# Kernel optimization log

Hardware: AMD Instinct MI355X
Metric: run time of the kernel (lower is better)

Reference implementation:

```python
import jax, jax.numpy as jnp
import numpy as np

B, S, HID = 1, 2048, 2048
NH, NKV, HD = 32, 8, 64  # query heads, kv heads, head dim
NEG = -1e9


def rotate_half(x):
    d = x.shape[-1] // 2
    return jnp.concatenate([-x[..., d:], x[..., :d]], axis=-1)


def setup_inputs() -> dict:
    key = jax.random.key(0)
    ks = jax.random.split(key, 8)
    hidden_states = jax.random.normal(ks[0], (B, S, HID), dtype=jnp.float32)
    # RoPE angles: realistic cos/sin tables (B, S, HD)
    inv_freq = 1.0 / (10000.0 ** (np.arange(0, HD, 2, dtype=np.float32) / HD))
    pos = np.arange(S, dtype=np.float32)
    ang = pos[:, None] * inv_freq[None, :]            # (S, HD/2)
    ang = np.concatenate([ang, ang], axis=-1)          # (S, HD)
    cos = jnp.broadcast_to(jnp.cos(ang)[None], (B, S, HD)).astype(jnp.float32)
    sin = jnp.broadcast_to(jnp.sin(ang)[None], (B, S, HD)).astype(jnp.float32)
    # additive causal mask (B, 1, S, S)
    causal = jnp.where(jnp.tril(jnp.ones((S, S), dtype=bool)), 0.0, NEG).astype(jnp.float32)
    attention_mask = jnp.broadcast_to(causal[None, None], (B, 1, S, S))
    std = 0.02
    Wq = jax.random.normal(ks[1], (NH * HD, HID), dtype=jnp.float32) * std
    Wk = jax.random.normal(ks[2], (NKV * HD, HID), dtype=jnp.float32) * std
    Wv = jax.random.normal(ks[3], (NKV * HD, HID), dtype=jnp.float32) * std
    Wo = jax.random.normal(ks[4], (HID, NH * HD), dtype=jnp.float32) * std
    return {"hidden_states": hidden_states, "cos": cos, "sin": sin,
            "attention_mask": attention_mask, "Wq": Wq, "Wk": Wk, "Wv": Wv, "Wo": Wo}


def reference(hidden_states, cos, sin, attention_mask, Wq, Wk, Wv, Wo):
    scaling = HD ** -0.5
    n_rep = NH // NKV
    # projections -> (B, H, S, D)
    q = jnp.einsum('bsh,qh->bsq', hidden_states, Wq).reshape(B, S, NH, HD).transpose(0, 2, 1, 3)
    k = jnp.einsum('bsh,qh->bsq', hidden_states, Wk).reshape(B, S, NKV, HD).transpose(0, 2, 1, 3)
    v = jnp.einsum('bsh,qh->bsq', hidden_states, Wv).reshape(B, S, NKV, HD).transpose(0, 2, 1, 3)
    # RoPE (cos/sin broadcast over head dim via [:, None])
    c, s = cos[:, None], sin[:, None]
    q = q * c + rotate_half(q) * s
    k = k * c + rotate_half(k) * s
    # GQA repeat_kv
    k = jnp.repeat(k, n_rep, axis=1)
    v = jnp.repeat(v, n_rep, axis=1)
    # eager attention
    attn_weights = jnp.einsum('bhqd,bhkd->bhqk', q, k) * scaling
    attn_weights = attn_weights + attention_mask
    attn_weights = jax.nn.softmax(attn_weights.astype(jnp.float32), axis=-1).astype(q.dtype)
    attn_output = jnp.einsum('bhqk,bhkd->bhqd', attn_weights, v)
    attn_output = attn_output.transpose(0, 2, 1, 3).reshape(B, S, NH * HD)
    attn_output = jnp.einsum('bsq,hq->bsh', attn_output, Wo)
    return attn_output, attn_weights
```

## Files before the change

### kernel.cpp

```cpp
#include <hip/hip_runtime.h>

#define S_LEN 2048
#define NH 32
#define NKV 8
#define HD 64
#define QH_DIM (NH * HD)
#define QKV_DIM 3072
#define K_OFF 2048
#define V_OFF 2560
#define LOG2E 1.44269504089f

typedef __attribute__((ext_vector_type(8))) __bf16 bf16x8;
typedef __attribute__((ext_vector_type(4))) float fx4;
typedef __attribute__((ext_vector_type(8))) unsigned short ush8;

__device__ __forceinline__ unsigned short f2bf(float f) {
  return __builtin_bit_cast(unsigned short, (__bf16)f);
}
__device__ __forceinline__ float bf2f(unsigned short h) {
  unsigned int u = ((unsigned int)h) << 16;
  return __builtin_bit_cast(float, u);
}
__device__ __forceinline__ fx4 zero4() {
  fx4 z; z[0] = 0.f; z[1] = 0.f; z[2] = 0.f; z[3] = 0.f; return z;
}

#define MFMA16(a, b, c) __builtin_amdgcn_mfma_f32_16x16x32_bf16((a), (b), (c), 0, 0, 0)

__device__ __forceinline__ void gl16(const void* g, void* l) {
  __builtin_amdgcn_global_load_lds((const __attribute__((address_space(1))) void*)g,
                                   (__attribute__((address_space(3))) void*)l, 16, 0, 0);
}

__global__ __launch_bounds__(256) void cast5(const float* __restrict__ s0, unsigned short* d0, int n0,
                                             const float* __restrict__ s1, unsigned short* d1, int n1,
                                             const float* __restrict__ s2, unsigned short* d2, int n2,
                                             const float* __restrict__ s3, unsigned short* d3, int n3,
                                             const float* __restrict__ s4, unsigned short* d4, int n4) {
  int i = blockIdx.x * 256 + threadIdx.x;
  const float* s;
  unsigned short* d;
  if (i < n0) { s = s0; d = d0; }
  else if ((i -= n0) < n1) { s = s1; d = d1; }
  else if ((i -= n1) < n2) { s = s2; d = d2; }
  else if ((i -= n2) < n3) { s = s3; d = d3; }
  else if ((i -= n3) < n4) { s = s4; d = d4; }
  else return;
  float4 v = ((const float4*)s)[i];
  ushort4 o;
  o.x = f2bf(v.x); o.y = f2bf(v.y); o.z = f2bf(v.z); o.w = f2bf(v.w);
  ((ushort4*)d)[i] = o;
}

__global__ __launch_bounds__(512, 6) void gemm_split(const unsigned short* __restrict__ A,
                                                     const unsigned short* __restrict__ B,
                                                     unsigned short* __restrict__ Part,
                                                     int M, int N, int K) {
  __shared__ unsigned short As[2][128 * 32];
  __shared__ unsigned short Bs[2][128 * 32];
  const int tid = threadIdx.x;
  const int bn = blockIdx.x * 128, bm = blockIdx.y * 128;
  const int kslice = blockIdx.z;
  const int KH = K >> 1;
  const size_t koff = (size_t)kslice * KH;
  const int lane = tid & 63, wid = tid >> 6;
  const int lo = lane & 15, g = lane >> 4;
  const int wr = wid >> 2, wc = wid & 3;

  fx4 acc[4][2];
#pragma unroll
  for (int i = 0; i < 4; i++)
#pragma unroll
    for (int j = 0; j < 2; j++) acc[i][j] = zero4();

  const int srow = tid >> 2;
  const int cg = (tid & 3) ^ ((srow >> 1) & 3);
  const unsigned short* apg = &A[(size_t)(bm + srow) * K + koff + cg * 8];
  const unsigned short* bpg = &B[(size_t)(bn + srow) * K + koff + cg * 8];

  const int arow = wr * 64 + lo;
  const int brow = wc * 32 + lo;
  const int sc = (g ^ ((lo >> 1) & 3)) * 8;

#define G_STAGE(s, k0)                  \
  do {                                  \
    gl16(apg + (k0), &As[s][tid * 8]);  \
    gl16(bpg + (k0), &Bs[s][tid * 8]);  \
  } while (0)

#define G_COMPUTE(s)                                                   \
  do {                                                                 \
    bf16x8 af[4], bb[2];                                               \
    _Pragma("unroll") for (int mi = 0; mi < 4; mi++)                   \
        af[mi] = *(const bf16x8*)&As[s][(arow + mi * 16) * 32 + sc];   \
    _Pragma("unroll") for (int nj = 0; nj < 2; nj++)                   \
        bb[nj] = *(const bf16x8*)&Bs[s][(brow + nj * 16) * 32 + sc];   \
    _Pragma("unroll") for (int mi = 0; mi < 4; mi++)                   \
        _Pragma("unroll") for (int nj = 0; nj < 2; nj++)               \
            acc[mi][nj] = MFMA16(af[mi], bb[nj], acc[mi][nj]);         \
  } while (0)

  const int NT = KH >> 5;
  G_STAGE(0, 0);
  __syncthreads();
  int cur = 0;
  for (int t = 0; t < NT - 1; ++t) {
    G_STAGE(cur ^ 1, (t + 1) * 32);
    G_COMPUTE(cur);
    __syncthreads();
    cur ^= 1;
  }
  G_COMPUTE(cur);
#undef G_STAGE
#undef G_COMPUTE

  unsigned short* const pb = &Part[(size_t)kslice * M * N];
#pragma unroll
  for (int mi = 0; mi < 4; mi++)
#pragma unroll
    for (int nj = 0; nj < 2; nj++)
#pragma unroll
      for (int r = 0; r < 4; r++) {
        int row = bm + wr * 64 + mi * 16 + g * 4 + r;
        int col = bn + wc * 32 + nj * 16 + lo;
        pb[(size_t)row * N + col] = f2bf(acc[mi][nj][r]);
      }
}

__global__ __launch_bounds__(256) void combine_qkv(const unsigned short* __restrict__ P0,
                                                   const unsigned short* __restrict__ P1,
                                                   unsigned short* __restrict__ qkv,
                                                   const float* __restrict__ cosp,
                                                   const float* __restrict__ sinp,
                                                   unsigned short* __restrict__ Vt) {
  __shared__ unsigned short t[64][72];
  const int b = blockIdx.x;
  if (b < 2560) {
    int idx = b * 256 + threadIdx.x;
    int j = idx & 7;
    int tt = idx >> 3;
    int head = tt % 40;
    int s = tt / 40;
    const float scale = (head < 32) ? 0.125f * LOG2E : 1.0f;
    const size_t base = (size_t)s * QKV_DIM + head * 64 + j * 4;
    ushort4 a0l = *(const ushort4*)&P0[base];
    ushort4 a1l = *(const ushort4*)&P1[base];
    ushort4 a0h = *(const ushort4*)&P0[base + 32];
    ushort4 a1h = *(const ushort4*)&P1[base + 32];
    float xl0 = bf2f(a0l.x) + bf2f(a1l.x), xl1 = bf2f(a0l.y) + bf2f(a1l.y);
    float xl2 = bf2f(a0l.z) + bf2f(a1l.z), xl3 = bf2f(a0l.w) + bf2f(a1l.w);
    float xh0 = bf2f(a0h.x) + bf2f(a1h.x), xh1 = bf2f(a0h.y) + bf2f(a1h.y);
    float xh2 = bf2f(a0h.z) + bf2f(a1h.z), xh3 = bf2f(a0h.w) + bf2f(a1h.w);
    fx4 cl = *(const fx4*)&cosp[s * 64 + j * 4];
    fx4 ch = *(const fx4*)&cosp[s * 64 + 32 + j * 4];
    fx4 sl = *(const fx4*)&sinp[s * 64 + j * 4];
    fx4 sh = *(const fx4*)&sinp[s * 64 + 32 + j * 4];
    ushort4 ol, oh;
    ol.x = f2bf((xl0 * cl[0] - xh0 * sl[0]) * scale);
    ol.y = f2bf((xl1 * cl[1] - xh1 * sl[1]) * scale);
    ol.z = f2bf((xl2 * cl[2] - xh2 * sl[2]) * scale);
    ol.w = f2bf((xl3 * cl[3] - xh3 * sl[3]) * scale);
    oh.x = f2bf((xh0 * ch[0] + xl0 * sh[0]) * scale);
    oh.y = f2bf((xh1 * ch[1] + xl1 * sh[1]) * scale);
    oh.z = f2bf((xh2 * ch[2] + xl2 * sh[2]) * scale);
    oh.w = f2bf((xh3 * ch[3] + xl3 * sh[3]) * scale);
    *(ushort4*)&qkv[base] = ol;
    *(ushort4*)&qkv[base + 32] = oh;
  } else {
    const int tid = threadIdx.x;
    const int bb = b - 2560;
    const int cb = (bb & 7) * 64;
    const int rb = (bb >> 3) * 64;
#pragma unroll
    for (int rr = 0; rr < 2; rr++) {
      int row = rr * 32 + (tid >> 3);
      int c8 = (tid & 7) * 8;
      const size_t src = (size_t)(rb + row) * QKV_DIM + V_OFF + cb + c8;
      ush8 a = *(const ush8*)&P0[src];
      ush8 c = *(const ush8*)&P1[src];
      ush8 o;
#pragma unroll
      for (int j = 0; j < 8; j++) o[j] = f2bf(bf2f(a[j]) + bf2f(c[j]));
      *(ush8*)&t[row][c8] = o;
    }
    __syncthreads();
#pragma unroll
    for (int rr = 0; rr < 2; rr++) {
      int col = rr * 32 + (tid >> 3);
      int r8 = (tid & 7) * 8;
      ush8 o;
#pragma unroll
      for (int j = 0; j < 8; j++) o[j] = t[r8 + j][col];
      *(ush8*)&Vt[(size_t)(cb + col) * S_LEN + rb + r8] = o;
    }
  }
}

__global__ __launch_bounds__(256) void combine_wo(const unsigned short* __restrict__ P0,
                                                  const unsigned short* __restrict__ P1,
                                                  float* __restrict__ out) {
  const int i = blockIdx.x * 256 + threadIdx.x;
  const size_t base = (size_t)i * 8;
  ush8 a = *(const ush8*)&P0[base];
  ush8 b = *(const ush8*)&P1[base];
  fx4 o0, o1;
#pragma unroll
  for (int j = 0; j < 4; j++) o0[j] = bf2f(a[j]) + bf2f(b[j]);
#pragma unroll
  for (int j = 0; j < 4; j++) o1[j] = bf2f(a[4 + j]) + bf2f(b[4 + j]);
  *(fx4*)&out[base] = o0;
  *(fx4*)&out[base + 4] = o1;
}

__global__ __launch_bounds__(512, 4) void attn_kernel(const unsigned short* __restrict__ Q,
                                                      const unsigned short* __restrict__ Kb,
                                                      const unsigned short* __restrict__ Vt,
                                                      float* __restrict__ P,
                                                      unsigned short* __restrict__ AO) {
  __shared__ unsigned short pls[16][2048];
  __shared__ float lred[8][16];
  __shared__ fx4 obuf[4][64];
  const int h = blockIdx.x;
  const int rt = 127 - blockIdx.y;
  const int hkv = h >> 2;
  const int wid = threadIdx.x >> 6, lane = threadIdx.x & 63;
  const int lo = lane & 15, g = lane >> 4;
  const int rowb = rt * 16;
  const int nkt = (rt + 4) >> 2;
  const int qg = rowb + lo;
  char* const plsb = (char*)pls;
  const int swz = (lo & 7) << 4;

  {
    const int zc0 = nkt * 64;
    const int nz4 = (S_LEN - zc0) >> 2;
    for (int idx = threadIdx.x; idx < 16 * nz4; idx += 512) {
      const int r = idx / nz4;
      const int c = idx - r * nz4;
      __builtin_nontemporal_store(zero4(),
          (fx4*)&P[((size_t)h * S_LEN + rowb + r) * S_LEN + zc0 + c * 4]);
    }
  }

  const bf16x8 qa0 = *(const bf16x8*)&Q[(size_t)qg * QKV_DIM + h * HD + g * 8];
  const bf16x8 qa1 = *(const bf16x8*)&Q[(size_t)qg * QKV_DIM + h * HD + 32 + g * 8];

  float l = 0.f;
  {
    bf16x8 kc0[4], kc1[4];
    if (wid < nkt) {
#pragma unroll
      for (int nj = 0; nj < 4; nj++) {
        const int kcol = wid * 64 + nj * 16 + lo;
        kc0[nj] = *(const bf16x8*)&Kb[(size_t)kcol * QKV_DIM + hkv * HD + g * 8];
        kc1[nj] = *(const bf16x8*)&Kb[(size_t)kcol * QKV_DIM + hkv * HD + 32 + g * 8];
      }
    }
    for (int kt = wid; kt < nkt; kt += 8) {
      bf16x8 kn0[4], kn1[4];
      if (kt + 8 < nkt) {
#pragma unroll
        for (int nj = 0; nj < 4; nj++) {
          const int kcol = (kt + 8) * 64 + nj * 16 + lo;
          kn0[nj] = *(const bf16x8*)&Kb[(size_t)kcol * QKV_DIM + hkv * HD + g * 8];
          kn1[nj] = *(const bf16x8*)&Kb[(size_t)kcol * QKV_DIM + hkv * HD + 32 + g * 8];
        }
      }
      fx4 acc[4];
      __builtin_amdgcn_s_setprio(1);
#pragma unroll
      for (int nj = 0; nj < 4; nj++) {
        acc[nj] = MFMA16(kc0[nj], qa0, zero4());
        acc[nj] = MFMA16(kc1[nj], qa1, acc[nj]);
      }
      __builtin_amdgcn_s_setprio(0);
      const bool diag = (kt == nkt - 1);
#pragma unroll
      for (int nj = 0; nj < 4; nj++) {
        float e[4];
#pragma unroll
        for (int r = 0; r < 4; r++) {
          float v = exp2f(acc[nj][r]);
          if (diag && (kt * 64 + nj * 16 + g * 4 + r > qg)) v = 0.f;
          l += v;
          e[r] = v;
        }
        unsigned int w0 = (unsigned int)f2bf(e[0]) | ((unsigned int)f2bf(e[1]) << 16);
        unsigned int w1 = (unsigned int)f2bf(e[2]) | ((unsigned int)f2bf(e[3]) << 16);
        uint2 w; w.x = w0; w.y = w1;
        *(uint2*)(plsb + lo * 4096 + ((kt * 128 + nj * 32 + g * 8) ^ swz)) = w;
      }
#pragma unroll
      for (int j = 0; j < 4; j++) { kc0[j] = kn0[j]; kc1[j] = kn1[j]; }
    }
  }
  l += __shfl_xor(l, 16);
  l += __shfl_xor(l, 32);
  if (lane < 16) lred[wid][lo] = l;

  const int d0 = (wid & 3) * 16;
  const int par = wid >> 2;
  const unsigned short* const vrow = &Vt[(size_t)(hkv * HD + d0 + lo) * S_LEN];
  bf16x8 vc0 = *(const bf16x8*)&vrow[par * 64 + g * 8];
  bf16x8 vc1 = *(const bf16x8*)&vrow[par * 64 + 32 + g * 8];

  __syncthreads();

  float pinv[4];
#pragma unroll
  for (int it = 0; it < 4; it++) {
    const int rho = it * 4 + g;
    pinv[it] = 1.f / (lred[0][rho] + lred[1][rho] + lred[2][rho] + lred[3][rho] +
                      lred[4][rho] + lred[5][rho] + lred[6][rho] + lred[7][rho]);
  }
  float* const pbase = &P[((size_t)h * S_LEN + rowb) * S_LEN];

  fx4 oacc = zero4();
  for (int kt = par; kt < nkt; kt += 2) {
    bf16x8 vn0, vn1;
    if (kt + 2 < nkt) {
      vn0 = *(const bf16x8*)&vrow[(kt + 2) * 64 + g * 8];
      vn1 = *(const bf16x8*)&vrow[(kt + 2) * 64 + 32 + g * 8];
    }
    bf16x8 pa0 = *(const bf16x8*)(plsb + lo * 4096 + ((kt * 128 + g * 16) ^ swz));
    bf16x8 pa1 = *(const bf16x8*)(plsb + lo * 4096 + ((kt * 128 + 64 + g * 16) ^ swz));
    __builtin_amdgcn_s_setprio(1);
    oacc = MFMA16(pa0, vc0, oacc);
    oacc = MFMA16(pa1, vc1, oacc);
    __builtin_amdgcn_s_setprio(0);
    if (((kt >> 1) & 3) == (wid & 3)) {
#pragma unroll
      for (int it = 0; it < 4; it++) {
        const int rho = it * 4 + g;
        ushort4 b4 = *(const ushort4*)(plsb + rho * 4096 +
                                       ((kt * 128 + lo * 8) ^ ((rho & 7) << 4)));
        fx4 pv;
        pv[0] = bf2f(b4.x) * pinv[it]; pv[1] = bf2f(b4.y) * pinv[it];
        pv[2] = bf2f(b4.z) * pinv[it]; pv[3] = bf2f(b4.w) * pinv[it];
        __builtin_nontemporal_store(pv,
            (fx4*)&pbase[(size_t)rho * S_LEN + kt * 64 + lo * 4]);
      }
    }
    vc0 = vn0; vc1 = vn1;
  }

  if (par == 1) obuf[wid & 3][lane] = oacc;
  __syncthreads();
  if (par == 0) {
    fx4 o2 = obuf[wid][lane];
#pragma unroll
    for (int r = 0; r < 4; r++) {
      const int q = g * 4 + r;
      const float linv = 1.f / (lred[0][q] + lred[1][q] + lred[2][q] + lred[3][q] +
                                lred[4][q] + lred[5][q] + lred[6][q] + lred[7][q]);
      AO[(size_t)(rowb + q) * QH_DIM + h * HD + d0 + lo] = f2bf((oacc[r] + o2[r]) * linv);
    }
  }
}

extern "C" void kernel_launch(void* const* d_in, const int* in_sizes, int n_in,
                              void* d_out, int out_size, void* d_ws, size_t ws_size,
                              hipStream_t stream) {
  const float* hs = (const float*)d_in[0];
  const float* cosp = (const float*)d_in[1];
  const float* sinp = (const float*)d_in[2];
  const float* Wq = (const float*)d_in[4];
  const float* Wk = (const float*)d_in[5];
  const float* Wv = (const float*)d_in[6];
  const float* Wo = (const float*)d_in[7];

  char* w = (char*)d_ws;
  unsigned short* wo_bf   = (unsigned short*)(w);
  unsigned short* ao_bf   = (unsigned short*)(w + (((size_t)9) << 20));
  unsigned short* hs_bf   = (unsigned short*)(w + (((size_t)18) << 20));
  unsigned short* wqkv_bf = (unsigned short*)(w + (((size_t)27) << 20));
  unsigned short* qkv_bf  = (unsigned short*)(w + (((size_t)40) << 20));
  unsigned short* vt_bf   = (unsigned short*)(w + (((size_t)53) << 20));
  unsigned short* wop     = hs_bf;

  float* out0 = (float*)d_out;
  float* P = out0 + (size_t)S_LEN * QH_DIM;
  const size_t P_BYTES = (size_t)NH * S_LEN * S_LEN * 4;
  const size_t QKVP_BYTES = (size_t)2 * S_LEN * QKV_DIM * 2;
  unsigned short* qkvp = (unsigned short*)((char*)P + P_BYTES - QKVP_BYTES);

  cast5<<<14336, 256, 0, stream>>>(hs, hs_bf, 1048576,
                                   Wq, wqkv_bf, 1048576,
                                   Wk, wqkv_bf + (size_t)K_OFF * 2048, 262144,
                                   Wv, wqkv_bf + (size_t)V_OFF * 2048, 262144,
                                   Wo, wo_bf, 1048576);

  gemm_split<<<dim3(QKV_DIM / 128, 16, 2), 512, 0, stream>>>(hs_bf, wqkv_bf, qkvp,
                                                             2048, QKV_DIM, 2048);

  combine_qkv<<<2816, 256, 0, stream>>>(qkvp, qkvp + (size_t)S_LEN * QKV_DIM,
                                        qkv_bf, cosp, sinp, vt_bf);

  attn_kernel<<<dim3(NH, 128), 512, 0, stream>>>(qkv_bf, qkv_bf + K_OFF, vt_bf, P, ao_bf);

  gemm_split<<<dim3(16, 16, 2), 512, 0, stream>>>(ao_bf, wo_bf, wop, 2048, 2048, 2048);

  combine_wo<<<2048, 256, 0, stream>>>(wop, wop + (size_t)S_LEN * QH_DIM, out0);
}
```

Baseline: 253.5 us.

## Fuse PV MFMA into score loop and split P writeback by key tile

The attention kernel now accumulates P·V inside the same per-wave key-tile loop that computes exp scores. Each wave covers all 64 head dims for its own key tiles, loading V directly from global memory, instead of running a second pass split by head-dim quarter and parity. The normalized P writeback becomes a separate loop over each wave's key tiles. The eight per-wave partial outputs are reduced through shared memory that reuses the P buffer, which replaces the old obuf. This removes a serialized second phase, at the cost of more accumulator registers and an 8-way reduction. The gemm K-split half size also becomes a kernel argument.

New measurement: 254.0 us. About the same (+0.2%).

```diff
diff --git a/kernel.cpp b/kernel.cpp
--- a/kernel.cpp
+++ b/kernel.cpp
@@ -55,13 +55,12 @@
 __global__ __launch_bounds__(512, 6) void gemm_split(const unsigned short* __restrict__ A,
                                                      const unsigned short* __restrict__ B,
                                                      unsigned short* __restrict__ Part,
-                                                     int M, int N, int K) {
+                                                     int M, int N, int K, int KH) {
   __shared__ unsigned short As[2][128 * 32];
   __shared__ unsigned short Bs[2][128 * 32];
   const int tid = threadIdx.x;
   const int bn = blockIdx.x * 128, bm = blockIdx.y * 128;
   const int kslice = blockIdx.z;
-  const int KH = K >> 1;
   const size_t koff = (size_t)kslice * KH;
   const int lane = tid & 63, wid = tid >> 6;
   const int lo = lane & 15, g = lane >> 4;
@@ -217,9 +216,8 @@
                                                       const unsigned short* __restrict__ Vt,
                                                       float* __restrict__ P,
                                                       unsigned short* __restrict__ AO) {
-  __shared__ unsigned short pls[16][2048];
+  __shared__ __align__(16) unsigned short pls[16][2048];
   __shared__ float lred[8][16];
-  __shared__ fx4 obuf[4][64];
   const int h = blockIdx.x;
   const int rt = 127 - blockIdx.y;
   const int hkv = h >> 2;
@@ -246,6 +244,10 @@
   const bf16x8 qa1 = *(const bf16x8*)&Q[(size_t)qg * QKV_DIM + h * HD + 32 + g * 8];
 
   float l = 0.f;
+  fx4 oacc[4];
+#pragma unroll
+  for (int dj = 0; dj < 4; dj++) oacc[dj] = zero4();
+
   {
     bf16x8 kc0[4], kc1[4];
     if (wid < nkt) {
@@ -291,18 +293,24 @@
         *(uint2*)(plsb + lo * 4096 + ((kt * 128 + nj * 32 + g * 8) ^ swz)) = w;
       }
 #pragma unroll
+      for (int kk = 0; kk < 2; kk++) {
+        bf16x8 pa = *(const bf16x8*)(plsb + lo * 4096 + ((kt * 128 + kk * 64 + g * 16) ^ swz));
+        __builtin_amdgcn_s_setprio(1);
+#pragma unroll
+        for (int dj = 0; dj < 4; dj++) {
+          bf16x8 vb = *(const bf16x8*)&Vt[(size_t)(hkv * HD + dj * 16 + lo) * S_LEN +
+                                          kt * 64 + kk * 32 + g * 8];
+          oacc[dj] = MFMA16(pa, vb, oacc[dj]);
+        }
+        __builtin_amdgcn_s_setprio(0);
+      }
+#pragma unroll
       for (int j = 0; j < 4; j++) { kc0[j] = kn0[j]; kc1[j] = kn1[j]; }
     }
   }
   l += __shfl_xor(l, 16);
   l += __shfl_xor(l, 32);
   if (lane < 16) lred[wid][lo] = l;
-
-  const int d0 = (wid & 3) * 16;
-  const int par = wid >> 2;
-  const unsigned short* const vrow = &Vt[(size_t)(hkv * HD + d0 + lo) * S_LEN];
-  bf16x8 vc0 = *(const bf16x8*)&vrow[par * 64 + g * 8];
-  bf16x8 vc1 = *(const bf16x8*)&vrow[par * 64 + 32 + g * 8];
 
   __syncthreads();
 
@@ -315,45 +323,39 @@
   }
   float* const pbase = &P[((size_t)h * S_LEN + rowb) * S_LEN];
 
-  fx4 oacc = zero4();
-  for (int kt = par; kt < nkt; kt += 2) {
-    bf16x8 vn0, vn1;
-    if (kt + 2 < nkt) {
-      vn0 = *(const bf16x8*)&vrow[(kt + 2) * 64 + g * 8];
-      vn1 = *(const bf16x8*)&vrow[(kt + 2) * 64 + 32 + g * 8];
-    }
-    bf16x8 pa0 = *(const bf16x8*)(plsb + lo * 4096 + ((kt * 128 + g * 16) ^ swz));
-    bf16x8 pa1 = *(const bf16x8*)(plsb + lo * 4096 + ((kt * 128 + 64 + g * 16) ^ swz));
-    __builtin_amdgcn_s_setprio(1);
-    oacc = MFMA16(pa0, vc0, oacc);
-    oacc = MFMA16(pa1, vc1, oacc);
-    __builtin_amdgcn_s_setprio(0);
-    if (((kt >> 1) & 3) == (wid & 3)) {
-#pragma unroll
-      for (int it = 0; it < 4; it++) {
-        const int rho = it * 4 + g;
-        ushort4 b4 = *(const ushort4*)(plsb + rho * 4096 +
-                                       ((kt * 128 + lo * 8) ^ ((rho & 7) << 4)));
-        fx4 pv;
-        pv[0] = bf2f(b4.x) * pinv[it]; pv[1] = bf2f(b4.y) * pinv[it];
-        pv[2] = bf2f(b4.z) * pinv[it]; pv[3] = bf2f(b4.w) * pinv[it];
-        __builtin_nontemporal_store(pv,
-            (fx4*)&pbase[(size_t)rho * S_LEN + kt * 64 + lo * 4]);
-      }
-    }
-    vc0 = vn0; vc1 = vn1;
-  }
-
-  if (par == 1) obuf[wid & 3][lane] = oacc;
+  for (int kt = wid; kt < nkt; kt += 8) {
+#pragma unroll
+    for (int it = 0; it < 4; it++) {
+      const int rho = it * 4 + g;
+      ushort4 b4 = *(const ushort4*)(plsb + rho * 4096 +
+                                     ((kt * 128 + lo * 8) ^ ((rho & 7) << 4)));
+      fx4 pv;
+      pv[0] = bf2f(b4.x) * pinv[it]; pv[1] = bf2f(b4.y) * pinv[it];
+      pv[2] = bf2f(b4.z) * pinv[it]; pv[3] = bf2f(b4.w) * pinv[it];
+      __builtin_nontemporal_store(pv,
+          (fx4*)&pbase[(size_t)rho * S_LEN + kt * 64 + lo * 4]);
+    }
+  }
+
   __syncthreads();
-  if (par == 0) {
-    fx4 o2 = obuf[wid][lane];
+  fx4* const obp = (fx4*)plsb;
+#pragma unroll
+  for (int dj = 0; dj < 4; dj++) obp[wid * 256 + dj * 64 + lane] = oacc[dj];
+  __syncthreads();
+  if (wid < 4) {
+    fx4 s = obp[wid * 64 + lane];
+#pragma unroll
+    for (int ww = 1; ww < 8; ww++) {
+      fx4 t2 = obp[ww * 256 + wid * 64 + lane];
+#pragma unroll
+      for (int j = 0; j < 4; j++) s[j] += t2[j];
+    }
 #pragma unroll
     for (int r = 0; r < 4; r++) {
       const int q = g * 4 + r;
       const float linv = 1.f / (lred[0][q] + lred[1][q] + lred[2][q] + lred[3][q] +
                                 lred[4][q] + lred[5][q] + lred[6][q] + lred[7][q]);
-      AO[(size_t)(rowb + q) * QH_DIM + h * HD + d0 + lo] = f2bf((oacc[r] + o2[r]) * linv);
+      AO[(size_t)(rowb + q) * QH_DIM + h * HD + wid * 16 + lo] = f2bf(s[r] * linv);
     }
   }
 }
@@ -391,14 +393,14 @@
                                    Wo, wo_bf, 1048576);
 
   gemm_split<<<dim3(QKV_DIM / 128, 16, 2), 512, 0, stream>>>(hs_bf, wqkv_bf, qkvp,
-                                                             2048, QKV_DIM, 2048);
+                                                             2048, QKV_DIM, 2048, 1024);
 
   combine_qkv<<<2816, 256, 0, stream>>>(qkvp, qkvp + (size_t)S_LEN * QKV_DIM,
                                         qkv_bf, cosp, sinp, vt_bf);
 
   attn_kernel<<<dim3(NH, 128), 512, 0, stream>>>(qkv_bf, qkv_bf + K_OFF, vt_bf, P, ao_bf);
 
-  gemm_split<<<dim3(16, 16, 2), 512, 0, stream>>>(ao_bf, wo_bf, wop, 2048, 2048, 2048);
+  gemm_split<<<dim3(16, 16, 2), 512, 0, stream>>>(ao_bf, wo_bf, wop, 2048, 2048, 2048, 1024);
 
   combine_wo<<<2048, 256, 0, stream>>>(wop, wop + (size_t)S_LEN * QH_DIM, out0);
 }
```
